# Optimization experiments

Measured on AMD Instinct MI355X. Metric: run time of the kernel, lower is better.

The kernel has to match this reference:

```python
import jax, jax.numpy as jnp
import numpy as np

V, E, H, S, B = 32000, 512, 1024, 256, 128
D_WIN = 5.0  # local attention half-window D


def setup_inputs() -> dict:
    key = jax.random.key(0)
    ks = jax.random.split(key, 12)
    f32 = jnp.float32
    nrm = lambda k, shape, s=0.02: (s * jax.random.normal(k, shape, dtype=f32))
    x = jax.random.randint(ks[0], (1, B), 0, V)  # single decode step of token ids
    previous_hidden = jax.random.normal(ks[1], (1, B, H), dtype=f32)
    encoder_outputs = jax.random.normal(ks[2], (S, B, H), dtype=f32)
    lengths = jax.random.randint(ks[3], (B,), S // 2, S + 1)
    enc_masks = (jnp.arange(S)[:, None] < lengths[None, :]).astype(jnp.int32)  # (S,B)
    emb = nrm(ks[4], (V, E))
    W_dec = nrm(ks[5], (H, H)); b_dec = jnp.zeros((H,), f32)
    W_pos = nrm(ks[6], (H, H)); b_pos = jnp.zeros((H,), f32)
    w_proj = nrm(ks[7], (1, H))
    W_ih = nrm(ks[8], (3 * H, E + H)); b_ih = jnp.zeros((3 * H,), f32)
    W_hh = nrm(ks[9], (3 * H, H)); b_hh = jnp.zeros((3 * H,), f32)
    W_fc = nrm(ks[10], (V, E + 2 * H)); b_fc = jnp.zeros((V,), f32)
    return dict(x=x, previous_hidden=previous_hidden, encoder_outputs=encoder_outputs,
                enc_masks=enc_masks, emb=emb, W_dec=W_dec, b_dec=b_dec,
                W_pos=W_pos, b_pos=b_pos, w_proj=w_proj,
                W_ih=W_ih, b_ih=b_ih, W_hh=W_hh, b_hh=b_hh, W_fc=W_fc, b_fc=b_fc)


def reference(x, previous_hidden, encoder_outputs, enc_masks, emb, W_dec, b_dec,
              W_pos, b_pos, w_proj, W_ih, b_ih, W_hh, b_hh, W_fc, b_fc):
    src_len = encoder_outputs.shape[0]
    x_emb = emb[x]                                   # (1,B,E); dropout is eval-mode identity
    phd = previous_hidden[-1]                        # (B,H)

    # per-batch encoder lengths: first index where mask==0, 0 -> full length
    src_lens = jnp.argmin(enc_masks.T, axis=1)
    src_lens = jnp.where(src_lens == 0, src_len, src_lens).astype(jnp.float32)  # (B,)

    # local (Luong-style) alignment scores: tanh of dot(dec, enc)
    dw = phd @ W_dec.T + b_dec                       # (B,H)
    energy = jnp.tanh(jnp.einsum('bh,sbh->sb', dw, encoder_outputs))  # (S,B)
    scores = jnp.where(enc_masks == 0, -jnp.inf, energy)
    att_w = jax.nn.softmax(scores, axis=0)           # (S,B)

    # predicted center position pt = (len-1) * sigmoid(v^T tanh(W_p h))
    t = jnp.tanh(previous_hidden @ W_pos.T + b_pos)  # (1,B,H)
    f_ht = jax.nn.sigmoid(t @ w_proj.T)[0, :, 0]     # (B,)
    pt = (src_lens - 1.0) * f_ht                     # (B,)

    # Gaussian window centered at pt, sigma = D/2, plus hard [pmin,pmax) mask
    s = jnp.arange(src_len, dtype=jnp.float32)[:, None]          # (S,1)
    sigma = D_WIN / 2.0
    window = jnp.exp(-((pt[None, :] - s) ** 2) / (2.0 * sigma ** 2))  # (S,B)
    pmax = jnp.floor(pt + D_WIN)
    pmin = jnp.floor(jnp.maximum(pt - D_WIN, 0.0))
    hard = (s < pmax[None, :]) & (s >= pmin[None, :])
    window = window * hard.astype(window.dtype)
    w = att_w * window                               # (S,B), NOT renormalized (as in source)

    context = jnp.einsum('sb,sbh->bh', w, encoder_outputs)  # (B,H)

    # single GRU step (torch gate order: r, z, n)
    gru_in = jnp.concatenate([x_emb[0], context], axis=1)    # (B,E+H)
    gi = gru_in @ W_ih.T + b_ih                              # (B,3H)
    gh = phd @ W_hh.T + b_hh                                 # (B,3H)
    i_r, i_z, i_n = jnp.split(gi, 3, axis=1)
    h_r, h_z, h_n = jnp.split(gh, 3, axis=1)
    r = jax.nn.sigmoid(i_r + h_r)
    zg = jax.nn.sigmoid(i_z + h_z)
    n = jnp.tanh(i_n + r * h_n)
    h_new = (1.0 - zg) * n + zg * phd                        # (B,H)

    new_input = jnp.concatenate([x_emb, h_new[None], context[None]], axis=2)  # (1,B,E+2H)
    z = new_input @ W_fc.T + b_fc                            # (1,B,V)
    return z, h_new[None]
```

## Files before the change

### kernel.cpp

```cpp
#include <hip/hip_runtime.h>
#include <math.h>

#define B_ 128
#define S_ 256
#define H_ 1024
#define E_ 512
#define V_ 32000
#define KZ (E_ + 2 * H_)

typedef short s8v  __attribute__((ext_vector_type(8)));
typedef float f32x4 __attribute__((ext_vector_type(4)));
typedef unsigned short us4 __attribute__((ext_vector_type(4)));
typedef unsigned short us8 __attribute__((ext_vector_type(8)));

__device__ __forceinline__ unsigned short f2bf(float f)
{
    union { float f; unsigned u; } v; v.f = f;
    unsigned r = v.u + 0x7fffu + ((v.u >> 16) & 1u);
    return (unsigned short)(r >> 16);
}

__global__ __launch_bounds__(256) void embed_kernel(const int* __restrict__ x,
                                                    const float* __restrict__ emb,
                                                    float* __restrict__ x_emb)
{
    int idx = blockIdx.x * 256 + threadIdx.x;
    int b = idx >> 9;
    int e = idx & 511;
    x_emb[idx] = emb[(size_t)x[b] * E_ + e];
}

__global__ __launch_bounds__(256) void bias_init(float* __restrict__ C,
                                                 const float* __restrict__ bias, int N)
{
    int idx = blockIdx.x * 256 + threadIdx.x;
    int n = idx % N;
    C[idx] = bias[n];
}

template<int TILE_N, int MICRO_N, bool ATOMIC>
__device__ __forceinline__ void gemm_core(const float* __restrict__ A,
                                          const float* __restrict__ W,
                                          const float* __restrict__ bias,
                                          float* __restrict__ C,
                                          int N, int K, int kbeg, int kend,
                                          float (*As)[132], float (*Ws)[TILE_N + 4])
{
    constexpr int NT_N   = TILE_N / MICRO_N;
    constexpr int NT_M   = 256 / NT_N;
    constexpr int MICRO_M = 128 / NT_M;
    const int tid = threadIdx.x;
    const int n0  = blockIdx.x * TILE_N;
    const int tn  = (tid % NT_N) * MICRO_N;
    const int tm  = (tid / NT_N) * MICRO_M;

    float acc[MICRO_M][MICRO_N] = {};

    for (int k0 = kbeg; k0 < kend; k0 += 16) {
        #pragma unroll
        for (int r = 0; r < 2; r++) {
            int v  = tid + 256 * r;
            int m  = v >> 2;
            int kk = (v & 3) << 2;
            float4 a4 = *(const float4*)(A + (size_t)m * K + k0 + kk);
            As[kk + 0][m] = a4.x; As[kk + 1][m] = a4.y;
            As[kk + 2][m] = a4.z; As[kk + 3][m] = a4.w;
        }
        for (int v = tid; v < TILE_N * 4; v += 256) {
            int n  = v >> 2;
            int kk = (v & 3) << 2;
            float4 w4 = *(const float4*)(W + (size_t)(n0 + n) * K + k0 + kk);
            Ws[kk + 0][n] = w4.x; Ws[kk + 1][n] = w4.y;
            Ws[kk + 2][n] = w4.z; Ws[kk + 3][n] = w4.w;
        }
        __syncthreads();
        #pragma unroll
        for (int kk = 0; kk < 16; kk++) {
            float a[MICRO_M], w[MICRO_N];
            #pragma unroll
            for (int i = 0; i < MICRO_M; i++) a[i] = As[kk][tm + i];
            #pragma unroll
            for (int j = 0; j < MICRO_N; j++) w[j] = Ws[kk][tn + j];
            #pragma unroll
            for (int i = 0; i < MICRO_M; i++)
                #pragma unroll
                for (int j = 0; j < MICRO_N; j++)
                    acc[i][j] = fmaf(a[i], w[j], acc[i][j]);
        }
        __syncthreads();
    }

    #pragma unroll
    for (int i = 0; i < MICRO_M; i++) {
        #pragma unroll
        for (int j = 0; j < MICRO_N; j++) {
            size_t off = (size_t)(tm + i) * N + n0 + tn + j;
            if (ATOMIC) atomicAdd(C + off, acc[i][j]);
            else        C[off] = acc[i][j] + bias[n0 + tn + j];
        }
    }
}

__global__ __launch_bounds__(256) void gemm_dual(const float* A0, const float* W0, float* C0, int K0, int kc0,
                                                 const float* A1, const float* W1, float* C1, int K1, int kc1,
                                                 int N)
{
    __shared__ float As[16][132];
    __shared__ float Ws[16][36];
    if (blockIdx.z == 0)
        gemm_core<32, 2, true>(A0, W0, nullptr, C0, N, K0,
                               blockIdx.y * kc0, blockIdx.y * kc0 + kc0, As, Ws);
    else
        gemm_core<32, 2, true>(A1, W1, nullptr, C1, N, K1,
                               blockIdx.y * kc1, blockIdx.y * kc1 + kc1, As, Ws);
}

__global__ __launch_bounds__(256) void gemm_z_mfma(const unsigned short* __restrict__ A,
                                                   const float* __restrict__ W,
                                                   const float* __restrict__ bias,
                                                   float* __restrict__ C)
{
    __shared__ unsigned short As[128 * 40];
    __shared__ unsigned short Ws[64 * 40];

    const int tid  = threadIdx.x;
    const int n0   = blockIdx.x * 64;
    const int w    = tid >> 6;
    const int lane = tid & 63;
    const int quad = lane >> 4;
    const int l16  = lane & 15;

    f32x4 acc[8] = {};

    for (int k0 = 0; k0 < KZ; k0 += 32) {
        #pragma unroll
        for (int r = 0; r < 2; r++) {
            int idx = tid + 256 * r;
            int m   = idx >> 2;
            int kk  = (idx & 3) << 3;
            *(us8*)&As[m * 40 + kk] = *(const us8*)(A + (size_t)m * KZ + k0 + kk);
        }
        #pragma unroll
        for (int r = 0; r < 2; r++) {
            int idx = tid + 256 * r;
            int n   = idx >> 3;
            int kk  = (idx & 7) << 2;
            float4 wv = *(const float4*)(W + (size_t)(n0 + n) * KZ + k0 + kk);
            us4 p; p.x = f2bf(wv.x); p.y = f2bf(wv.y); p.z = f2bf(wv.z); p.w = f2bf(wv.w);
            *(us4*)&Ws[n * 40 + kk] = p;
        }
        __syncthreads();

        s8v bfrag = *(const s8v*)&Ws[(w * 16 + l16) * 40 + quad * 8];
        #pragma unroll
        for (int mt = 0; mt < 8; mt++) {
            s8v afrag = *(const s8v*)&As[(mt * 16 + l16) * 40 + quad * 8];
            acc[mt] = __builtin_amdgcn_mfma_f32_16x16x32_bf16(afrag, bfrag, acc[mt], 0, 0, 0);
        }
        __syncthreads();
    }

    const int n  = n0 + w * 16 + l16;
    const float bv = bias[n];
    #pragma unroll
    for (int mt = 0; mt < 8; mt++) {
        #pragma unroll
        for (int r = 0; r < 4; r++) {
            int m = mt * 16 + quad * 4 + r;
            C[(size_t)m * V_ + n] = acc[mt][r] + bv;
        }
    }
}

__global__ __launch_bounds__(256) void pt_kernel(const int* __restrict__ masks,
                                                 const float* __restrict__ dwpos,
                                                 const float* __restrict__ w_proj,
                                                 float* __restrict__ pt)
{
    __shared__ int   smin_s[4];
    __shared__ float ssum[4];
    int b = blockIdx.x, tid = threadIdx.x;
    int lane = tid & 63, wv = tid >> 6;

    int first = (masks[tid * B_ + b] == 0) ? tid : S_;
    for (int off = 32; off; off >>= 1) first = min(first, __shfl_down(first, off, 64));
    if (lane == 0) smin_s[wv] = first;

    float sum = 0.f;
    for (int i = tid; i < H_; i += 256) sum += w_proj[i] * tanhf(dwpos[(size_t)b * H_ + i]);
    for (int off = 32; off; off >>= 1) sum += __shfl_down(sum, off, 64);
    if (lane == 0) ssum[wv] = sum;
    __syncthreads();
    if (tid == 0) {
        int   fz  = min(min(smin_s[0], smin_s[1]), min(smin_s[2], smin_s[3]));
        float tot = ssum[0] + ssum[1] + ssum[2] + ssum[3];
        float fht = 1.f / (1.f + expf(-tot));
        pt[b] = ((float)fz - 1.f) * fht;
    }
}

__global__ __launch_bounds__(256) void energy_kernel(const float* __restrict__ dw,
                                                     const float* __restrict__ enc,
                                                     const int* __restrict__ masks,
                                                     float* __restrict__ energy)
{
    int wid  = (blockIdx.x << 2) + (threadIdx.x >> 6);
    int lane = threadIdx.x & 63;
    int b    = wid & (B_ - 1);
    const float4* ep = (const float4*)(enc + (size_t)wid * H_);
    const float4* dp = (const float4*)(dw + (size_t)b * H_);
    float acc = 0.f;
    #pragma unroll
    for (int i = 0; i < 4; i++) {
        float4 a = dp[lane + (i << 6)];
        float4 e = ep[lane + (i << 6)];
        acc += a.x * e.x + a.y * e.y + a.z * e.z + a.w * e.w;
    }
    for (int off = 32; off; off >>= 1) acc += __shfl_down(acc, off, 64);
    if (lane == 0)
        energy[wid] = masks[wid] ? tanhf(acc) : -1e30f;
}

__global__ __launch_bounds__(256) void softmax_window(const float* __restrict__ energy,
                                                      const float* __restrict__ pt,
                                                      float* __restrict__ w_sb)
{
    __shared__ float sred[4];
    int b = blockIdx.x, s = threadIdx.x;
    int lane = s & 63, wv = s >> 6;
    float e = energy[s * B_ + b];

    float m = e;
    for (int off = 32; off; off >>= 1) m = fmaxf(m, __shfl_down(m, off, 64));
    if (lane == 0) sred[wv] = m;
    __syncthreads();
    m = fmaxf(fmaxf(sred[0], sred[1]), fmaxf(sred[2], sred[3]));
    __syncthreads();

    float ex = expf(e - m);
    float l = ex;
    for (int off = 32; off; off >>= 1) l += __shfl_down(l, off, 64);
    if (lane == 0) sred[wv] = l;
    __syncthreads();
    l = sred[0] + sred[1] + sred[2] + sred[3];

    float aw   = ex / l;
    float ptb  = pt[b];
    float fs   = (float)s;
    float pmax = floorf(ptb + 5.f);
    float pmin = floorf(fmaxf(ptb - 5.f, 0.f));
    float d    = ptb - fs;
    float win  = ((fs < pmax) && (fs >= pmin)) ? expf(-(d * d) * (1.f / 12.5f)) : 0.f;
    w_sb[s * B_ + b] = aw * win;
}

__global__ __launch_bounds__(256) void context_kernel(const float* __restrict__ w_sb,
                                                      const float* __restrict__ enc,
                                                      const float* __restrict__ pt,
                                                      float* __restrict__ ctx)
{
    int b = blockIdx.y;
    int h = blockIdx.x * 256 + threadIdx.x;
    float ptb = pt[b];
    int smin = (int)floorf(fmaxf(ptb - 5.f, 0.f));
    int smax = min((int)floorf(ptb + 5.f), S_);
    float acc = 0.f;
    for (int s = smin; s < smax; s++)
        acc += w_sb[s * B_ + b] * enc[(size_t)(s * B_ + b) * H_ + h];
    ctx[(size_t)b * H_ + h] = acc;
}

__global__ __launch_bounds__(256) void concat_gru_in(const float* __restrict__ x_emb,
                                                     const float* __restrict__ ctx,
                                                     float* __restrict__ gru_in)
{
    int idx = blockIdx.x * 256 + threadIdx.x;
    int b = idx / (E_ + H_);
    int k = idx - b * (E_ + H_);
    gru_in[idx] = (k < E_) ? x_emb[b * E_ + k] : ctx[(size_t)b * H_ + k - E_];
}

__global__ __launch_bounds__(256) void concat_new_input(const float* __restrict__ x_emb,
                                                        const float* __restrict__ h_new,
                                                        const float* __restrict__ ctx,
                                                        unsigned short* __restrict__ ni)
{
    int idx = blockIdx.x * 256 + threadIdx.x;
    int b = idx / (E_ + 2 * H_);
    int k = idx - b * (E_ + 2 * H_);
    float v;
    if (k < E_)            v = x_emb[b * E_ + k];
    else if (k < E_ + H_)  v = h_new[(size_t)b * H_ + k - E_];
    else                   v = ctx[(size_t)b * H_ + k - E_ - H_];
    ni[idx] = f2bf(v);
}

__global__ __launch_bounds__(256) void gru_kernel(const float* __restrict__ gi,
                                                  const float* __restrict__ gh,
                                                  const float* __restrict__ phd,
                                                  float* __restrict__ h_new,
                                                  float* __restrict__ out_h)
{
    int idx = blockIdx.x * 256 + threadIdx.x;
    int b = idx >> 10;
    int i = idx & 1023;
    const float* gib = gi + (size_t)b * 3 * H_;
    const float* ghb = gh + (size_t)b * 3 * H_;
    float ir = gib[i], iz = gib[H_ + i], in_ = gib[2 * H_ + i];
    float hr = ghb[i], hz = ghb[H_ + i], hn  = ghb[2 * H_ + i];
    float r  = 1.f / (1.f + expf(-(ir + hr)));
    float zg = 1.f / (1.f + expf(-(iz + hz)));
    float n  = tanhf(in_ + r * hn);
    float h  = (1.f - zg) * n + zg * phd[idx];
    h_new[idx] = h;
    out_h[idx] = h;
}

extern "C" void kernel_launch(void* const* d_in, const int* in_sizes, int n_in,
                              void* d_out, int out_size, void* d_ws, size_t ws_size,
                              hipStream_t stream)
{
    const int*   x      = (const int*)  d_in[0];
    const float* phd    = (const float*)d_in[1];
    const float* enc    = (const float*)d_in[2];
    const int*   masks  = (const int*)  d_in[3];
    const float* emb    = (const float*)d_in[4];
    const float* W_dec  = (const float*)d_in[5];
    const float* b_dec  = (const float*)d_in[6];
    const float* W_pos  = (const float*)d_in[7];
    const float* b_pos  = (const float*)d_in[8];
    const float* w_proj = (const float*)d_in[9];
    const float* W_ih   = (const float*)d_in[10];
    const float* b_ih   = (const float*)d_in[11];
    const float* W_hh   = (const float*)d_in[12];
    const float* b_hh   = (const float*)d_in[13];
    const float* W_fc   = (const float*)d_in[14];
    const float* b_fc   = (const float*)d_in[15];

    float* out_z = (float*)d_out;
    float* out_h = out_z + (size_t)B_ * V_;

    float* ws       = (float*)d_ws;
    float* x_emb    = ws;  ws += B_ * E_;
    float* dwdec    = ws;  ws += B_ * H_;
    float* dwpos    = ws;  ws += B_ * H_;
    float* pt       = ws;  ws += 128;
    float* energy   = ws;  ws += S_ * B_;
    float* w_sb     = ws;  ws += S_ * B_;
    float* ctx      = ws;  ws += B_ * H_;
    float* gru_in   = ws;  ws += B_ * (E_ + H_);
    float* gi       = ws;  ws += B_ * 3 * H_;
    float* gh       = ws;  ws += B_ * 3 * H_;
    float* h_new    = ws;  ws += B_ * H_;
    unsigned short* n_in_bf = (unsigned short*)ws;

    embed_kernel<<<B_ * E_ / 256, 256, 0, stream>>>(x, emb, x_emb);

    bias_init<<<B_ * H_ / 256, 256, 0, stream>>>(dwdec, b_dec, H_);
    bias_init<<<B_ * H_ / 256, 256, 0, stream>>>(dwpos, b_pos, H_);
    gemm_dual<<<dim3(H_ / 32, 4, 2), 256, 0, stream>>>(phd, W_dec, dwdec, H_, 256,
                                                       phd, W_pos, dwpos, H_, 256, H_);

    pt_kernel<<<B_, 256, 0, stream>>>(masks, dwpos, w_proj, pt);
    energy_kernel<<<S_ * B_ / 4, 256, 0, stream>>>(dwdec, enc, masks, energy);
    softmax_window<<<B_, 256, 0, stream>>>(energy, pt, w_sb);
    context_kernel<<<dim3(H_ / 256, B_), 256, 0, stream>>>(w_sb, enc, pt, ctx);

    concat_gru_in<<<B_ * (E_ + H_) / 256, 256, 0, stream>>>(x_emb, ctx, gru_in);
    bias_init<<<B_ * 3 * H_ / 256, 256, 0, stream>>>(gi, b_ih, 3 * H_);
    bias_init<<<B_ * 3 * H_ / 256, 256, 0, stream>>>(gh, b_hh, 3 * H_);
    gemm_dual<<<dim3(3 * H_ / 32, 4, 2), 256, 0, stream>>>(gru_in, W_ih, gi, E_ + H_, 384,
                                                           phd,    W_hh, gh, H_,      256, 3 * H_);

    gru_kernel<<<B_ * H_ / 256, 256, 0, stream>>>(gi, gh, phd, h_new, out_h);
    concat_new_input<<<B_ * (E_ + 2 * H_) / 256, 256, 0, stream>>>(x_emb, h_new, ctx, n_in_bf);

    gemm_z_mfma<<<V_ / 64, 256, 0, stream>>>(n_in_bf, W_fc, b_fc, out_z);
}
```

Before: 705.9 us.

## Fuse prep/concat kernels and pipeline W_fc loads in output GEMM

Merges the embedding gather and the four bias-init launches into one prep kernel. It folds the gru_in concat into the GRU-input GEMM's A loads, and fuses the GRU cell with the new_input concat. That concat now writes bf16 directly in MFMA fragment order. The vocab GEMM reads A fragments straight from global memory instead of staging them in LDS, and software-pipelines the W_fc loads with register double buffering and a 4-deep LDS ring, so there is one barrier per k-step. The aim is fewer launches and intermediate buffers, plus hiding W_fc load latency in the dominant GEMM, at the cost of more complex indexing and redundant per-block global reads of A.

```diff
diff --git a/kernel.cpp b/kernel.cpp
--- a/kernel.cpp
+++ b/kernel.cpp
@@ -7,6 +7,7 @@
 #define E_ 512
 #define V_ 32000
 #define KZ (E_ + 2 * H_)
+#define NKB (KZ / 32)
 
 typedef short s8v  __attribute__((ext_vector_type(8)));
 typedef float f32x4 __attribute__((ext_vector_type(4)));
@@ -20,26 +21,29 @@
     return (unsigned short)(r >> 16);
 }
 
-__global__ __launch_bounds__(256) void embed_kernel(const int* __restrict__ x,
-                                                    const float* __restrict__ emb,
-                                                    float* __restrict__ x_emb)
+__global__ __launch_bounds__(256) void prep_kernel(
+    const int* __restrict__ x, const float* __restrict__ emb, float* __restrict__ x_emb,
+    const float* __restrict__ b_dec, float* __restrict__ dwdec,
+    const float* __restrict__ b_pos, float* __restrict__ dwpos,
+    const float* __restrict__ b_ih, float* __restrict__ gi,
+    const float* __restrict__ b_hh, float* __restrict__ gh)
 {
     int idx = blockIdx.x * 256 + threadIdx.x;
-    int b = idx >> 9;
-    int e = idx & 511;
-    x_emb[idx] = emb[(size_t)x[b] * E_ + e];
-}
-
-__global__ __launch_bounds__(256) void bias_init(float* __restrict__ C,
-                                                 const float* __restrict__ bias, int N)
-{
-    int idx = blockIdx.x * 256 + threadIdx.x;
-    int n = idx % N;
-    C[idx] = bias[n];
-}
-
-template<int TILE_N, int MICRO_N, bool ATOMIC>
+    if (idx < B_ * E_) { x_emb[idx] = emb[(size_t)x[idx >> 9] * E_ + (idx & 511)]; return; }
+    idx -= B_ * E_;
+    if (idx < B_ * H_) { dwdec[idx] = b_dec[idx & 1023]; return; }
+    idx -= B_ * H_;
+    if (idx < B_ * H_) { dwpos[idx] = b_pos[idx & 1023]; return; }
+    idx -= B_ * H_;
+    if (idx < B_ * 3 * H_) { gi[idx] = b_ih[idx % (3 * H_)]; return; }
+    idx -= B_ * 3 * H_;
+    gh[idx] = b_hh[idx % (3 * H_)];
+}
+
+template<int TILE_N, int MICRO_N, bool ATOMIC, bool CONCAT>
 __device__ __forceinline__ void gemm_core(const float* __restrict__ A,
+                                          const float* __restrict__ Aa,
+                                          const float* __restrict__ Ab,
                                           const float* __restrict__ W,
                                           const float* __restrict__ bias,
                                           float* __restrict__ C,
@@ -62,7 +66,13 @@
             int v  = tid + 256 * r;
             int m  = v >> 2;
             int kk = (v & 3) << 2;
-            float4 a4 = *(const float4*)(A + (size_t)m * K + k0 + kk);
+            int kcol = k0 + kk;
+            float4 a4;
+            if (CONCAT)
+                a4 = (kcol < E_) ? *(const float4*)(Aa + (size_t)m * E_ + kcol)
+                                 : *(const float4*)(Ab + (size_t)m * H_ + (kcol - E_));
+            else
+                a4 = *(const float4*)(A + (size_t)m * K + kcol);
             As[kk + 0][m] = a4.x; As[kk + 1][m] = a4.y;
             As[kk + 2][m] = a4.z; As[kk + 3][m] = a4.w;
         }
@@ -101,27 +111,28 @@
     }
 }
 
-__global__ __launch_bounds__(256) void gemm_dual(const float* A0, const float* W0, float* C0, int K0, int kc0,
+template<bool CONCAT0>
+__global__ __launch_bounds__(256) void gemm_dual(const float* A0, const float* A0a, const float* A0b,
+                                                 const float* W0, float* C0, int K0, int kc0,
                                                  const float* A1, const float* W1, float* C1, int K1, int kc1,
                                                  int N)
 {
     __shared__ float As[16][132];
     __shared__ float Ws[16][36];
     if (blockIdx.z == 0)
-        gemm_core<32, 2, true>(A0, W0, nullptr, C0, N, K0,
-                               blockIdx.y * kc0, blockIdx.y * kc0 + kc0, As, Ws);
+        gemm_core<32, 2, true, CONCAT0>(A0, A0a, A0b, W0, nullptr, C0, N, K0,
+                                        blockIdx.y * kc0, blockIdx.y * kc0 + kc0, As, Ws);
     else
-        gemm_core<32, 2, true>(A1, W1, nullptr, C1, N, K1,
-                               blockIdx.y * kc1, blockIdx.y * kc1 + kc1, As, Ws);
-}
-
-__global__ __launch_bounds__(256) void gemm_z_mfma(const unsigned short* __restrict__ A,
+        gemm_core<32, 2, true, false>(A1, nullptr, nullptr, W1, nullptr, C1, N, K1,
+                                      blockIdx.y * kc1, blockIdx.y * kc1 + kc1, As, Ws);
+}
+
+__global__ __launch_bounds__(256) void gemm_z_mfma(const unsigned short* __restrict__ A2,
                                                    const float* __restrict__ W,
                                                    const float* __restrict__ bias,
                                                    float* __restrict__ C)
 {
-    __shared__ unsigned short As[128 * 40];
-    __shared__ unsigned short Ws[64 * 40];
+    __shared__ unsigned short Ws[4][64 * 40];
 
     const int tid  = threadIdx.x;
     const int n0   = blockIdx.x * 64;
@@ -130,46 +141,65 @@
     const int quad = lane >> 4;
     const int l16  = lane & 15;
 
+    const int sn0 = tid >> 3;
+    const int sk  = (tid & 7) << 2;
+    const float* wp0 = W + (size_t)(n0 + sn0) * KZ + sk;
+    const float* wp1 = W + (size_t)(n0 + sn0 + 32) * KZ + sk;
+    const int wsoff0 = sn0 * 40 + sk;
+    const int wsoff1 = (sn0 + 32) * 40 + sk;
+    const unsigned short* ap = A2 + lane * 8;
+    const int boff = (w * 16 + l16) * 40 + quad * 8;
+
+    float4 wA[2], wB[2];
     f32x4 acc[8] = {};
 
-    for (int k0 = 0; k0 < KZ; k0 += 32) {
-        #pragma unroll
-        for (int r = 0; r < 2; r++) {
-            int idx = tid + 256 * r;
-            int m   = idx >> 2;
-            int kk  = (idx & 3) << 3;
-            *(us8*)&As[m * 40 + kk] = *(const us8*)(A + (size_t)m * KZ + k0 + kk);
-        }
-        #pragma unroll
-        for (int r = 0; r < 2; r++) {
-            int idx = tid + 256 * r;
-            int n   = idx >> 3;
-            int kk  = (idx & 7) << 2;
-            float4 wv = *(const float4*)(W + (size_t)(n0 + n) * KZ + k0 + kk);
-            us4 p; p.x = f2bf(wv.x); p.y = f2bf(wv.y); p.z = f2bf(wv.z); p.w = f2bf(wv.w);
-            *(us4*)&Ws[n * 40 + kk] = p;
-        }
-        __syncthreads();
-
-        s8v bfrag = *(const s8v*)&Ws[(w * 16 + l16) * 40 + quad * 8];
-        #pragma unroll
-        for (int mt = 0; mt < 8; mt++) {
-            s8v afrag = *(const s8v*)&As[(mt * 16 + l16) * 40 + quad * 8];
-            acc[mt] = __builtin_amdgcn_mfma_f32_16x16x32_bf16(afrag, bfrag, acc[mt], 0, 0, 0);
-        }
-        __syncthreads();
+    auto ldw = [&](int kb, float4 (&r)[2]) {
+        r[0] = *(const float4*)(wp0 + kb * 32);
+        r[1] = *(const float4*)(wp1 + kb * 32);
+    };
+    auto stw = [&](int buf, const float4 (&r)[2]) {
+        us4 p0, p1;
+        p0.x = f2bf(r[0].x); p0.y = f2bf(r[0].y); p0.z = f2bf(r[0].z); p0.w = f2bf(r[0].w);
+        p1.x = f2bf(r[1].x); p1.y = f2bf(r[1].y); p1.z = f2bf(r[1].z); p1.w = f2bf(r[1].w);
+        *(us4*)&Ws[buf][wsoff0] = p0;
+        *(us4*)&Ws[buf][wsoff1] = p1;
+    };
+    auto barrier = [&]() {
+        asm volatile("s_waitcnt lgkmcnt(0)" ::: "memory");
+        __builtin_amdgcn_s_barrier();
+        asm volatile("" ::: "memory");
+    };
+    auto subiter = [&](int kb, float4 (&wLd)[2], const float4 (&wSt)[2]) {
+        s8v af[8];
+        const unsigned short* ab = ap + (size_t)kb * 4096;
+        #pragma unroll
+        for (int mt = 0; mt < 8; mt++) af[mt] = *(const s8v*)(ab + mt * 512);
+        if (kb + 2 < NKB) ldw(kb + 2, wLd);
+        s8v bfrag = *(const s8v*)&Ws[kb & 3][boff];
+        #pragma unroll
+        for (int mt = 0; mt < 8; mt++)
+            acc[mt] = __builtin_amdgcn_mfma_f32_16x16x32_bf16(af[mt], bfrag, acc[mt], 0, 0, 0);
+        if (kb + 1 < NKB) stw((kb + 1) & 3, wSt);
+        barrier();
+    };
+
+    ldw(0, wA); ldw(1, wB);
+    stw(0, wA);
+    barrier();
+
+    #pragma unroll 1
+    for (int kb = 0; kb < NKB; kb += 2) {
+        subiter(kb,     wA, wB);
+        subiter(kb + 1, wB, wA);
     }
 
     const int n  = n0 + w * 16 + l16;
     const float bv = bias[n];
     #pragma unroll
-    for (int mt = 0; mt < 8; mt++) {
-        #pragma unroll
-        for (int r = 0; r < 4; r++) {
-            int m = mt * 16 + quad * 4 + r;
-            C[(size_t)m * V_ + n] = acc[mt][r] + bv;
-        }
-    }
+    for (int mt = 0; mt < 8; mt++)
+        #pragma unroll
+        for (int r = 0; r < 4; r++)
+            C[(size_t)(mt * 16 + quad * 4 + r) * V_ + n] = acc[mt][r] + bv;
 }
 
 __global__ __launch_bounds__(256) void pt_kernel(const int* __restrict__ masks,
@@ -270,50 +300,52 @@
     ctx[(size_t)b * H_ + h] = acc;
 }
 
-__global__ __launch_bounds__(256) void concat_gru_in(const float* __restrict__ x_emb,
-                                                     const float* __restrict__ ctx,
-                                                     float* __restrict__ gru_in)
-{
-    int idx = blockIdx.x * 256 + threadIdx.x;
-    int b = idx / (E_ + H_);
-    int k = idx - b * (E_ + H_);
-    gru_in[idx] = (k < E_) ? x_emb[b * E_ + k] : ctx[(size_t)b * H_ + k - E_];
-}
-
-__global__ __launch_bounds__(256) void concat_new_input(const float* __restrict__ x_emb,
-                                                        const float* __restrict__ h_new,
-                                                        const float* __restrict__ ctx,
-                                                        unsigned short* __restrict__ ni)
-{
-    int idx = blockIdx.x * 256 + threadIdx.x;
-    int b = idx / (E_ + 2 * H_);
-    int k = idx - b * (E_ + 2 * H_);
-    float v;
-    if (k < E_)            v = x_emb[b * E_ + k];
-    else if (k < E_ + H_)  v = h_new[(size_t)b * H_ + k - E_];
-    else                   v = ctx[(size_t)b * H_ + k - E_ - H_];
-    ni[idx] = f2bf(v);
-}
-
-__global__ __launch_bounds__(256) void gru_kernel(const float* __restrict__ gi,
+__global__ __launch_bounds__(256) void gru_concat(const float* __restrict__ x_emb,
+                                                  const float* __restrict__ gi,
                                                   const float* __restrict__ gh,
                                                   const float* __restrict__ phd,
-                                                  float* __restrict__ h_new,
-                                                  float* __restrict__ out_h)
-{
-    int idx = blockIdx.x * 256 + threadIdx.x;
-    int b = idx >> 10;
-    int i = idx & 1023;
-    const float* gib = gi + (size_t)b * 3 * H_;
-    const float* ghb = gh + (size_t)b * 3 * H_;
-    float ir = gib[i], iz = gib[H_ + i], in_ = gib[2 * H_ + i];
-    float hr = ghb[i], hz = ghb[H_ + i], hn  = ghb[2 * H_ + i];
-    float r  = 1.f / (1.f + expf(-(ir + hr)));
-    float zg = 1.f / (1.f + expf(-(iz + hz)));
-    float n  = tanhf(in_ + r * hn);
-    float h  = (1.f - zg) * n + zg * phd[idx];
-    h_new[idx] = h;
-    out_h[idx] = h;
+                                                  const float* __restrict__ ctx,
+                                                  float* __restrict__ out_h,
+                                                  unsigned short* __restrict__ A2)
+{
+    int gid = blockIdx.x * 256 + threadIdx.x;
+    int l   = gid & 63;
+    int mt  = (gid >> 6) & 7;
+    int kb  = gid >> 9;
+    int b   = mt * 16 + (l & 15);
+    int k0  = kb * 32 + ((l >> 4) << 3);
+
+    float v[8];
+    if (k0 < E_) {
+        const float* p = x_emb + (size_t)b * E_ + k0;
+        #pragma unroll
+        for (int j = 0; j < 8; j++) v[j] = p[j];
+    } else if (k0 < E_ + H_) {
+        int i0 = k0 - E_;
+        const float* gib = gi + (size_t)b * 3 * H_ + i0;
+        const float* ghb = gh + (size_t)b * 3 * H_ + i0;
+        const float* ph  = phd + (size_t)b * H_ + i0;
+        float* oh = out_h + (size_t)b * H_ + i0;
+        #pragma unroll
+        for (int j = 0; j < 8; j++) {
+            float ir = gib[j], iz = gib[H_ + j], in_ = gib[2 * H_ + j];
+            float hr = ghb[j], hz = ghb[H_ + j], hn  = ghb[2 * H_ + j];
+            float r  = 1.f / (1.f + expf(-(ir + hr)));
+            float zg = 1.f / (1.f + expf(-(iz + hz)));
+            float n  = tanhf(in_ + r * hn);
+            float h  = (1.f - zg) * n + zg * ph[j];
+            oh[j] = h;
+            v[j] = h;
+        }
+    } else {
+        const float* p = ctx + (size_t)b * H_ + (k0 - E_ - H_);
+        #pragma unroll
+        for (int j = 0; j < 8; j++) v[j] = p[j];
+    }
+    us8 o;
+    #pragma unroll
+    for (int j = 0; j < 8; j++) o[j] = f2bf(v[j]);
+    *(us8*)(A2 + (size_t)gid * 8) = o;
 }
 
 extern "C" void kernel_launch(void* const* d_in, const int* in_sizes, int n_in,
@@ -348,32 +380,27 @@
     float* energy   = ws;  ws += S_ * B_;
     float* w_sb     = ws;  ws += S_ * B_;
     float* ctx      = ws;  ws += B_ * H_;
-    float* gru_in   = ws;  ws += B_ * (E_ + H_);
     float* gi       = ws;  ws += B_ * 3 * H_;
     float* gh       = ws;  ws += B_ * 3 * H_;
-    float* h_new    = ws;  ws += B_ * H_;
-    unsigned short* n_in_bf = (unsigned short*)ws;
-
-    embed_kernel<<<B_ * E_ / 256, 256, 0, stream>>>(x, emb, x_emb);
-
-    bias_init<<<B_ * H_ / 256, 256, 0, stream>>>(dwdec, b_dec, H_);
-    bias_init<<<B_ * H_ / 256, 256, 0, stream>>>(dwpos, b_pos, H_);
-    gemm_dual<<<dim3(H_ / 32, 4, 2), 256, 0, stream>>>(phd, W_dec, dwdec, H_, 256,
-                                                       phd, W_pos, dwpos, H_, 256, H_);
+    unsigned short* A2 = (unsigned short*)ws;
+
+    prep_kernel<<<4352, 256, 0, stream>>>(x, emb, x_emb, b_dec, dwdec, b_pos, dwpos,
+                                          b_ih, gi, b_hh, gh);
+
+    gemm_dual<false><<<dim3(H_ / 32, 4, 2), 256, 0, stream>>>(
+        phd, nullptr, nullptr, W_dec, dwdec, H_, 256,
+        phd,                   W_pos, dwpos, H_, 256, H_);
 
     pt_kernel<<<B_, 256, 0, stream>>>(masks, dwpos, w_proj, pt);
     energy_kernel<<<S_ * B_ / 4, 256, 0, stream>>>(dwdec, enc, masks, energy);
     softmax_window<<<B_, 256, 0, stream>>>(energy, pt, w_sb);
     context_kernel<<<dim3(H_ / 256, B_), 256, 0, stream>>>(w_sb, enc, pt, ctx);
 
-    concat_gru_in<<<B_ * (E_ + H_) / 256, 256, 0, stream>>>(x_emb, ctx, gru_in);
-    bias_init<<<B_ * 3 * H_ / 256, 256, 0, stream>>>(gi, b_ih, 3 * H_);
-    bias_init<<<B_ * 3 * H_ / 256, 256, 0, stream>>>(gh, b_hh, 3 * H_);
-    gemm_dual<<<dim3(3 * H_ / 32, 4, 2), 256, 0, stream>>>(gru_in, W_ih, gi, E_ + H_, 384,
-                                                           phd,    W_hh, gh, H_,      256, 3 * H_);
-
-    gru_kernel<<<B_ * H_ / 256, 256, 0, stream>>>(gi, gh, phd, h_new, out_h);
-    concat_new_input<<<B_ * (E_ + 2 * H_) / 256, 256, 0, stream>>>(x_emb, h_new, ctx, n_in_bf);
-
-    gemm_z_mfma<<<V_ / 64, 256, 0, stream>>>(n_in_bf, W_fc, b_fc, out_z);
-}
+    gemm_dual<true><<<dim3(3 * H_ / 32, 4, 2), 256, 0, stream>>>(
+        nullptr, x_emb, ctx, W_ih, gi, E_ + H_, 384,
+        phd,                 W_hh, gh, H_,      256, 3 * H_);
+
+    gru_concat<<<B_ * KZ / 8 / 256, 256, 0, stream>>>(x_emb, gi, gh, phd, ctx, out_h, A2);
+
+    gemm_z_mfma<<<V_ / 64, 256, 0, stream>>>(A2, W_fc, b_fc, out_z);
+}
```

New measurement: 711.4 us. No clear change (+0.8%).
